# Kernel tuning notes

Measured on AMD Instinct MI355X. Metric: run time of the kernel, lower is better.

Reference implementation:

```python
import jax, jax.numpy as jnp
import numpy as np

D_MODEL = 1024
D_STATE = 64
CHUNK = 256
BATCH = 4
SEQ_LEN = 4096


def setup_inputs() -> dict:
    key = jax.random.key(0)
    k1, k2, k3, k4, k5 = jax.random.split(key, 5)
    u = jax.random.normal(k1, (BATCH, SEQ_LEN, D_MODEL), jnp.float32)
    delta = jax.random.uniform(k2, (BATCH, SEQ_LEN, D_MODEL), jnp.float32)
    B = jax.random.normal(k3, (BATCH, SEQ_LEN, D_STATE), jnp.float32)
    C = jax.random.normal(k4, (BATCH, SEQ_LEN, D_STATE), jnp.float32)
    # matches nn.init.uniform_(A_log, -3.0, -1.0)
    A_log = jax.random.uniform(k5, (D_STATE, D_MODEL), jnp.float32, minval=-3.0, maxval=-1.0)
    return {"u": u, "delta": delta, "B": B, "C": C, "A_log": A_log}


def reference(u, delta, B, C, A_log):
    # delta is accepted but unused, as in the original forward.
    batch, seq_len, d_model = u.shape
    d_state = A_log.shape[0]
    n_chunks = seq_len // CHUNK  # seq_len chosen divisible by chunk_size
    A = -jnp.exp(A_log)  # (N, D)

    # Split sequence into chunks; hidden state resets at each chunk boundary,
    # so all chunks scan independently (vectorized over the n_chunks axis).
    # time-major layout for lax.scan: (CHUNK, batch, n_chunks, ...)
    uc = jnp.moveaxis(u.reshape(batch, n_chunks, CHUNK, d_model), 2, 0)
    Bc = jnp.moveaxis(B.reshape(batch, n_chunks, CHUNK, d_state), 2, 0)
    Cc = jnp.moveaxis(C.reshape(batch, n_chunks, CHUNK, d_state), 2, 0)

    h0 = jnp.zeros((batch, n_chunks, d_state, d_model), u.dtype)

    def step(h, inp):
        x_t, B_t, C_t = inp  # (b,c,D), (b,c,N), (b,c,N)
        h = A * h + B_t[..., :, None] * x_t[..., None, :]  # (b,c,N,D)
        y = jnp.einsum('bcn,bcnd->bcd', C_t, h)             # (b,c,D)
        return h, y

    _, ys = jax.lax.scan(step, h0, (uc, Bc, Cc))  # (CHUNK, b, n_chunks, D)
    out = jnp.moveaxis(ys, 0, 2).reshape(batch, seq_len, d_model)
    return out
```

## Files before the change

kernel.cpp:

```cpp
#include <hip/hip_runtime.h>

typedef float v2f __attribute__((ext_vector_type(2)));

#define D_MODEL 1024
#define D_STATE 64
#define CHUNK   256
#define TILE_T  64

__global__ __launch_bounds__(256, 1)
void YvParallelScan_kernel(const float* __restrict__ u,
                           const float* __restrict__ B,
                           const float* __restrict__ C,
                           const float* __restrict__ A_log,
                           float* __restrict__ out) {
    __shared__ float4 sB4[TILE_T * 16];
    __shared__ float4 sC4[TILE_T * 16];

    const int bc = blockIdx.x >> 2;
    const int dq = blockIdx.x & 3;
    const int d  = dq * 256 + threadIdx.x;
    const int rowbase = bc * CHUNK;

    v2f a2[32], h2[32];
#pragma unroll
    for (int k = 0; k < 32; ++k) {
        float a0 = A_log[(size_t)(2 * k)     * D_MODEL + d];
        float a1 = A_log[(size_t)(2 * k + 1) * D_MODEL + d];
        v2f av; av.x = -__expf(a0); av.y = -__expf(a1);
        a2[k] = av;
        v2f z; z.x = 0.f; z.y = 0.f;
        h2[k] = z;
    }

    const float*  uptr = u   + (size_t)rowbase * D_MODEL + d;
    float*        optr = out + (size_t)rowbase * D_MODEL + d;
    const float4* Bg   = (const float4*)(B + (size_t)rowbase * D_STATE);
    const float4* Cg   = (const float4*)(C + (size_t)rowbase * D_STATE);

    float xa = uptr[0];
    float xb = uptr[D_MODEL];

    for (int ti = 0; ti < CHUNK / TILE_T; ++ti) {
        __syncthreads();
#pragma unroll
        for (int k = 0; k < 4; ++k) {
            int flat = threadIdx.x + k * 256;
            sB4[flat] = Bg[ti * (TILE_T * 16) + flat];
            sC4[flat] = Cg[ti * (TILE_T * 16) + flat];
        }
        __syncthreads();

#pragma unroll 2
        for (int tl = 0; tl < TILE_T; ++tl) {
            const int t  = ti * TILE_T + tl;
            const int tp = (t + 2 < CHUNK) ? (t + 2) : (CHUNK - 1);
            float xn = uptr[(size_t)tp * D_MODEL];

            v2f xx;   xx.x = xa;  xx.y = xa;
            v2f acc0; acc0.x = 0.f; acc0.y = 0.f;
            v2f acc1; acc1.x = 0.f; acc1.y = 0.f;

#pragma unroll
            for (int g = 0; g < 16; ++g) {
                float4 b4 = sB4[tl * 16 + g];
                float4 c4 = sC4[tl * 16 + g];
                v2f b01; b01.x = b4.x; b01.y = b4.y;
                v2f b23; b23.x = b4.z; b23.y = b4.w;
                v2f c01; c01.x = c4.x; c01.y = c4.y;
                v2f c23; c23.x = c4.z; c23.y = c4.w;

                h2[2 * g]     = a2[2 * g]     * h2[2 * g]     + b01 * xx;
                h2[2 * g + 1] = a2[2 * g + 1] * h2[2 * g + 1] + b23 * xx;
                acc0 += c01 * h2[2 * g];
                acc1 += c23 * h2[2 * g + 1];
            }

            optr[(size_t)t * D_MODEL] = (acc0.x + acc0.y) + (acc1.x + acc1.y);
            xa = xb;
            xb = xn;
        }
    }
}

extern "C" void kernel_launch(void* const* d_in, const int* in_sizes, int n_in,
                              void* d_out, int out_size, void* d_ws, size_t ws_size,
                              hipStream_t stream) {
    const float* u     = (const float*)d_in[0];
    const float* B     = (const float*)d_in[2];
    const float* C     = (const float*)d_in[3];
    const float* A_log = (const float*)d_in[4];
    float* out = (float*)d_out;

    YvParallelScan_kernel<<<256, 256, 0, stream>>>(u, B, C, A_log, out);
}
```

Baseline: 306.0 us.

## Use single-wavefront blocks with scalar B/C loads instead of LDS tiles

```diff
diff --git a/kernel.cpp b/kernel.cpp
--- a/kernel.cpp
+++ b/kernel.cpp
@@ -1,84 +1,67 @@
 #include <hip/hip_runtime.h>
-
-typedef float v2f __attribute__((ext_vector_type(2)));
 
 #define D_MODEL 1024
 #define D_STATE 64
 #define CHUNK   256
-#define TILE_T  64
 
-__global__ __launch_bounds__(256, 1)
+__global__ __launch_bounds__(64, 1)
 void YvParallelScan_kernel(const float* __restrict__ u,
                            const float* __restrict__ B,
                            const float* __restrict__ C,
                            const float* __restrict__ A_log,
                            float* __restrict__ out) {
-    __shared__ float4 sB4[TILE_T * 16];
-    __shared__ float4 sC4[TILE_T * 16];
-
-    const int bc = blockIdx.x >> 2;
-    const int dq = blockIdx.x & 3;
-    const int d  = dq * 256 + threadIdx.x;
+    const int bc = blockIdx.x >> 4;
+    const int dg = blockIdx.x & 15;
+    const int d  = dg * 64 + threadIdx.x;
     const int rowbase = bc * CHUNK;
 
-    v2f a2[32], h2[32];
+    float a[D_STATE], h[D_STATE];
 #pragma unroll
-    for (int k = 0; k < 32; ++k) {
-        float a0 = A_log[(size_t)(2 * k)     * D_MODEL + d];
-        float a1 = A_log[(size_t)(2 * k + 1) * D_MODEL + d];
-        v2f av; av.x = -__expf(a0); av.y = -__expf(a1);
-        a2[k] = av;
-        v2f z; z.x = 0.f; z.y = 0.f;
-        h2[k] = z;
+    for (int n = 0; n < D_STATE; ++n) {
+        a[n] = -__expf(A_log[n * D_MODEL + d]);
+        h[n] = 0.f;
     }
 
-    const float*  uptr = u   + (size_t)rowbase * D_MODEL + d;
-    float*        optr = out + (size_t)rowbase * D_MODEL + d;
-    const float4* Bg   = (const float4*)(B + (size_t)rowbase * D_STATE);
-    const float4* Cg   = (const float4*)(C + (size_t)rowbase * D_STATE);
+    const float* uptr = u   + (size_t)rowbase * D_MODEL + d;
+    float*       optr = out + (size_t)rowbase * D_MODEL + d;
+    const float* Brow = B   + (size_t)rowbase * D_STATE;
+    const float* Crow = C   + (size_t)rowbase * D_STATE;
 
     float xa = uptr[0];
     float xb = uptr[D_MODEL];
 
-    for (int ti = 0; ti < CHUNK / TILE_T; ++ti) {
-        __syncthreads();
-#pragma unroll
-        for (int k = 0; k < 4; ++k) {
-            int flat = threadIdx.x + k * 256;
-            sB4[flat] = Bg[ti * (TILE_T * 16) + flat];
-            sC4[flat] = Cg[ti * (TILE_T * 16) + flat];
-        }
-        __syncthreads();
+    for (int t = 0; t < CHUNK; ++t) {
+        const int tp = (t + 2 < CHUNK) ? (t + 2) : (CHUNK - 1);
+        float xn = uptr[(size_t)tp * D_MODEL];
 
-#pragma unroll 2
-        for (int tl = 0; tl < TILE_T; ++tl) {
-            const int t  = ti * TILE_T + tl;
-            const int tp = (t + 2 < CHUNK) ? (t + 2) : (CHUNK - 1);
-            float xn = uptr[(size_t)tp * D_MODEL];
-
-            v2f xx;   xx.x = xa;  xx.y = xa;
-            v2f acc0; acc0.x = 0.f; acc0.y = 0.f;
-            v2f acc1; acc1.x = 0.f; acc1.y = 0.f;
+        const float x = xa;
+        float acc0 = 0.f, acc1 = 0.f, acc2 = 0.f, acc3 = 0.f;
 
 #pragma unroll
-            for (int g = 0; g < 16; ++g) {
-                float4 b4 = sB4[tl * 16 + g];
-                float4 c4 = sC4[tl * 16 + g];
-                v2f b01; b01.x = b4.x; b01.y = b4.y;
-                v2f b23; b23.x = b4.z; b23.y = b4.w;
-                v2f c01; c01.x = c4.x; c01.y = c4.y;
-                v2f c23; c23.x = c4.z; c23.y = c4.w;
+        for (int n = 0; n < D_STATE; n += 4) {
+            float b0 = Brow[t * D_STATE + n + 0];
+            float b1 = Brow[t * D_STATE + n + 1];
+            float b2 = Brow[t * D_STATE + n + 2];
+            float b3 = Brow[t * D_STATE + n + 3];
+            float c0 = Crow[t * D_STATE + n + 0];
+            float c1 = Crow[t * D_STATE + n + 1];
+            float c2 = Crow[t * D_STATE + n + 2];
+            float c3 = Crow[t * D_STATE + n + 3];
 
-                h2[2 * g]     = a2[2 * g]     * h2[2 * g]     + b01 * xx;
-                h2[2 * g + 1] = a2[2 * g + 1] * h2[2 * g + 1] + b23 * xx;
-                acc0 += c01 * h2[2 * g];
-                acc1 += c23 * h2[2 * g + 1];
-            }
+            h[n + 0] = a[n + 0] * h[n + 0] + b0 * x;
+            h[n + 1] = a[n + 1] * h[n + 1] + b1 * x;
+            h[n + 2] = a[n + 2] * h[n + 2] + b2 * x;
+            h[n + 3] = a[n + 3] * h[n + 3] + b3 * x;
 
-            optr[(size_t)t * D_MODEL] = (acc0.x + acc0.y) + (acc1.x + acc1.y);
-            xa = xb;
-            xb = xn;
+            acc0 = fmaf(c0, h[n + 0], acc0);
+            acc1 = fmaf(c1, h[n + 1], acc1);
+            acc2 = fmaf(c2, h[n + 2], acc2);
+            acc3 = fmaf(c3, h[n + 3], acc3);
         }
+
+        optr[(size_t)t * D_MODEL] = (acc0 + acc1) + (acc2 + acc3);
+        xa = xb;
+        xb = xn;
     }
 }
 
@@ -91,5 +74,5 @@
     const float* A_log = (const float*)d_in[4];
     float* out = (float*)d_out;
 
-    YvParallelScan_kernel<<<256, 256, 0, stream>>>(u, B, C, A_log, out);
+    YvParallelScan_kernel<<<1024, 64, 0, stream>>>(u, B, C, A_log, out);
 }
```

New measurement: 485.5 us. 1.59x slower.

## Split state dimension across wavefronts with vectorized d and LDS reduction

Applied to the files above, without the earlier changes.

```diff
diff --git a/kernel.cpp b/kernel.cpp
--- a/kernel.cpp
+++ b/kernel.cpp
@@ -1,6 +1,6 @@
 #include <hip/hip_runtime.h>
 
-typedef float v2f __attribute__((ext_vector_type(2)));
+typedef float v4 __attribute__((ext_vector_type(4)));
 
 #define D_MODEL 1024
 #define D_STATE 64
@@ -13,71 +13,81 @@
                            const float* __restrict__ C,
                            const float* __restrict__ A_log,
                            float* __restrict__ out) {
-    __shared__ float4 sB4[TILE_T * 16];
-    __shared__ float4 sC4[TILE_T * 16];
+    __shared__ v4 sB[TILE_T * 16];
+    __shared__ v4 sC[TILE_T * 16];
+    __shared__ v4 sP[2][4][64];
 
-    const int bc = blockIdx.x >> 2;
-    const int dq = blockIdx.x & 3;
-    const int d  = dq * 256 + threadIdx.x;
+    const int bc   = blockIdx.x >> 2;
+    const int dq   = blockIdx.x & 3;
+    const int tid  = threadIdx.x;
+    const int ng   = tid >> 6;
+    const int lane = tid & 63;
     const int rowbase = bc * CHUNK;
 
-    v2f a2[32], h2[32];
+    const v4* Bg = (const v4*)(B + (size_t)rowbase * D_STATE);
+    const v4* Cg = (const v4*)(C + (size_t)rowbase * D_STATE);
+
+    const int dbase4 = dq * 64 + lane;
+
+    v4 a4[16], h4[16];
 #pragma unroll
-    for (int k = 0; k < 32; ++k) {
-        float a0 = A_log[(size_t)(2 * k)     * D_MODEL + d];
-        float a1 = A_log[(size_t)(2 * k + 1) * D_MODEL + d];
-        v2f av; av.x = -__expf(a0); av.y = -__expf(a1);
-        a2[k] = av;
-        v2f z; z.x = 0.f; z.y = 0.f;
-        h2[k] = z;
+    for (int j = 0; j < 16; ++j) {
+        const int n = ng * 16 + j;
+        v4 al = ((const v4*)A_log)[n * 256 + dbase4];
+        v4 na;
+        na[0] = -__expf(al[0]); na[1] = -__expf(al[1]);
+        na[2] = -__expf(al[2]); na[3] = -__expf(al[3]);
+        a4[j] = na;
+        v4 z = {0.f, 0.f, 0.f, 0.f};
+        h4[j] = z;
     }
 
-    const float*  uptr = u   + (size_t)rowbase * D_MODEL + d;
-    float*        optr = out + (size_t)rowbase * D_MODEL + d;
-    const float4* Bg   = (const float4*)(B + (size_t)rowbase * D_STATE);
-    const float4* Cg   = (const float4*)(C + (size_t)rowbase * D_STATE);
+    const v4* uptr = (const v4*)(u + (size_t)rowbase * D_MODEL) + dbase4;
+    v4*       optr = (v4*)(out + (size_t)rowbase * D_MODEL) + dbase4;
 
-    float xa = uptr[0];
-    float xb = uptr[D_MODEL];
+    v4 xa = uptr[0];
+    v4 xb = uptr[256];
 
     for (int ti = 0; ti < CHUNK / TILE_T; ++ti) {
-        __syncthreads();
 #pragma unroll
         for (int k = 0; k < 4; ++k) {
-            int flat = threadIdx.x + k * 256;
-            sB4[flat] = Bg[ti * (TILE_T * 16) + flat];
-            sC4[flat] = Cg[ti * (TILE_T * 16) + flat];
+            sB[k * 256 + tid] = Bg[ti * 1024 + k * 256 + tid];
+            sC[k * 256 + tid] = Cg[ti * 1024 + k * 256 + tid];
         }
         __syncthreads();
 
-#pragma unroll 2
+#pragma unroll 4
         for (int tl = 0; tl < TILE_T; ++tl) {
             const int t  = ti * TILE_T + tl;
             const int tp = (t + 2 < CHUNK) ? (t + 2) : (CHUNK - 1);
-            float xn = uptr[(size_t)tp * D_MODEL];
+            v4 xn = uptr[(size_t)tp * 256];
 
-            v2f xx;   xx.x = xa;  xx.y = xa;
-            v2f acc0; acc0.x = 0.f; acc0.y = 0.f;
-            v2f acc1; acc1.x = 0.f; acc1.y = 0.f;
-
+            const v4 x = xa;
+            v4 acc = {0.f, 0.f, 0.f, 0.f};
 #pragma unroll
-            for (int g = 0; g < 16; ++g) {
-                float4 b4 = sB4[tl * 16 + g];
-                float4 c4 = sC4[tl * 16 + g];
-                v2f b01; b01.x = b4.x; b01.y = b4.y;
-                v2f b23; b23.x = b4.z; b23.y = b4.w;
-                v2f c01; c01.x = c4.x; c01.y = c4.y;
-                v2f c23; c23.x = c4.z; c23.y = c4.w;
-
-                h2[2 * g]     = a2[2 * g]     * h2[2 * g]     + b01 * xx;
-                h2[2 * g + 1] = a2[2 * g + 1] * h2[2 * g + 1] + b23 * xx;
-                acc0 += c01 * h2[2 * g];
-                acc1 += c23 * h2[2 * g + 1];
+            for (int jj = 0; jj < 4; ++jj) {
+                v4 b4 = sB[tl * 16 + ng * 4 + jj];
+                v4 c4 = sC[tl * 16 + ng * 4 + jj];
+#pragma unroll
+                for (int k = 0; k < 4; ++k) {
+                    const int j = jj * 4 + k;
+                    h4[j] = a4[j] * h4[j] + b4[k] * x;
+                    acc  += c4[k] * h4[j];
+                }
             }
 
-            optr[(size_t)t * D_MODEL] = (acc0.x + acc0.y) + (acc1.x + acc1.y);
-            xa = xb;
-            xb = xn;
+            const int slot = t & 1;
+            const int red  = t & 3;
+            if (ng != red) sP[slot][ng][lane] = acc;
+            __syncthreads();
+            if (ng == red) {
+                v4 s = acc;
+#pragma unroll
+                for (int w = 0; w < 4; ++w)
+                    if (w != red) s += sP[slot][w][lane];
+                optr[(size_t)t * 256] = s;
+            }
+            xa = xb; xb = xn;
         }
     }
 }
```

Result: faster. 266.6 us (-12.9%).
